# Performance work log

Hardware: AMD Instinct MI355X
Metric: run time of the kernel (lower is better)

The kernel has to match this reference:

```python
import jax, jax.numpy as jnp
import numpy as np

LEAK = 0.01  # PyTorch LeakyReLU default negative_slope


def _leaky(x):
    return jnp.where(x >= 0, x, LEAK * x)


def _sim1(x, ws):
    # 7-layer 1x1-conv MLP applied per pixel; x: (..., Cin, H, W)
    n = len(ws)
    for i, w in enumerate(ws):
        x = jnp.einsum('oc,...chw->...ohw', w, x)
        if i < n - 1:
            x = _leaky(x)
    return x


def setup_inputs() -> dict:
    key = jax.random.key(0)
    ks = jax.random.split(key, 9)
    B, C, S, K = 8, 256, 15, 17
    d = {
        'template_feature': jax.random.normal(ks[0], (B, C, S, S), jnp.float32),
        'candidate_feature': jax.random.normal(ks[1], (B, C, S + K - 1, S + K - 1), jnp.float32),
    }
    chans = [(C, 2 * C), (C // 2, C), (C // 4, C // 2), (C // 8, C // 4),
             (C // 16, C // 8), (C // 32, C // 16), (1, C // 32)]
    for i, (o, c) in enumerate(chans):
        # kaiming_normal_ fan_out for a 1x1 conv: std = sqrt(2/out_channels)
        d[f'w{i}'] = jax.random.normal(ks[2 + i], (o, c), jnp.float32) * np.sqrt(2.0 / o).astype(np.float32)
    return d


def reference(template_feature, candidate_feature, w0, w1, w2, w3, w4, w5, w6):
    ws = (w0, w1, w2, w3, w4, w5, w6)
    B, C, S, _ = template_feature.shape
    K = 17  # sliding-window grid (31-15+1)

    # ---- template branch ----
    t_mean = jnp.mean(template_feature, axis=(-2, -1), keepdims=True)
    rep = jnp.concatenate([jnp.broadcast_to(t_mean, template_feature.shape),
                           template_feature], axis=1)  # (B, 2C, S, S)
    w = _sim1(rep, ws)  # (B, 1, S, S)
    wn = jax.nn.softmax(w.reshape(B, 1, -1), axis=2).reshape(B, 1, S, S)
    common_template = jnp.sum(template_feature * wn, axis=(-2, -1)).reshape(B, C, 1, 1)

    # ---- candidate branch: im2col of 15x15 windows over 31x31 -> 17x17 grid ----
    ii = jnp.arange(S)[:, None] + jnp.arange(K)[None, :]  # (S, K): in-window + window-offset
    # cand_all[b,c,i,j,p,q] = candidate[b,c, i+p, j+q]  -> (B, C, S, S, K, K)
    cand_all = candidate_feature[:, :, ii[:, None, :, None], ii[None, :, None, :]]
    c_mean = jnp.mean(cand_all, axis=(2, 3), keepdims=True)  # divide by S*S as in original
    rep_c = jnp.concatenate([jnp.broadcast_to(c_mean, cand_all.shape), cand_all], axis=1)  # (B, 2C, S, S, K, K)
    rep_c = jnp.transpose(rep_c, (0, 4, 5, 1, 2, 3))  # (B, K, K, 2C, S, S)
    w_c = _sim1(rep_c, ws)  # (B, K, K, 1, S, S)
    wcn = jax.nn.softmax(w_c.reshape(B, K, K, 1, -1), axis=-1).reshape(B, K, K, 1, S, S)
    wcn = jnp.transpose(wcn, (0, 3, 4, 5, 1, 2))  # (B, 1, S, S, K, K)
    common_candidate = jnp.sum(cand_all * wcn, axis=(2, 3))  # (B, C, K, K)

    return common_template, common_candidate
```

## Files before the change

kernel.cpp:

```cpp
#include <hip/hip_runtime.h>

typedef _Float16 half_t;
typedef half_t half4 __attribute__((ext_vector_type(4)));
typedef half_t half8 __attribute__((ext_vector_type(8)));
typedef __fp16 pk16x2 __attribute__((ext_vector_type(2)));
typedef float  f32x4 __attribute__((ext_vector_type(4)));
typedef float  f32x2 __attribute__((ext_vector_type(2)));

static __device__ __forceinline__ half4 pack4(f32x4 a) {
  pk16x2 lo = __builtin_amdgcn_cvt_pkrtz(a[0], a[1]);
  pk16x2 hi = __builtin_amdgcn_cvt_pkrtz(a[2], a[3]);
  half4 h;
  h[0] = lo[0]; h[1] = lo[1]; h[2] = hi[0]; h[3] = hi[1];
  return h;
}

constexpr int B_  = 8;
constexpr int S_  = 15;
constexpr int K_  = 17;
constexpr int P_  = 31;
constexpr int SS_ = 225;
constexpr int PP_ = 961;
constexpr int KK_ = 289;

constexpr int NROW_C = B_ * PP_;
constexpr int NROW_T = B_ * SS_;
constexpr int NROW   = NROW_C + NROW_T;

constexpr int NW0H = 512 * 256;
constexpr int NF16 = 128*256 + 64*128 + 32*64;

constexpr size_t OFF_IN   = 0;
constexpr size_t OFF_OUT0 = OFF_IN   + (size_t)NROW * 256;
constexpr size_t OFF_ROWS = OFF_OUT0 + (size_t)NROW * 512;
constexpr size_t OFF_M0   = OFF_ROWS + (size_t)B_ * 31 * 17 * 256;
constexpr size_t OFF_TM0  = OFF_M0   + (size_t)B_ * KK_ * 256;
constexpr size_t OFF_F16  = OFF_TM0  + (size_t)B_ * 256;

constexpr int X0B  = 0;
constexpr int X1B  = 32768;
constexpr int X3TB = 32768;
constexpr int Y4B  = 41984;
constexpr int SMB  = 49152;
constexpr int REDB = 50112;
constexpr int W4B  = 50176;
constexpr int W5B  = 52480;
constexpr int W6B  = 53120;
constexpr int ROWB = 53152;
constexpr int LDSB = 53632;

__global__ __launch_bounds__(256) void featT_kernel(
    const float* __restrict__ templ, const float* __restrict__ cand,
    float* __restrict__ inarr)
{
  __shared__ float tile[32 * 257];
  const int bid = blockIdx.x;
  const float* src;
  int base, npos, rowbase;
  if (bid < B_ * 31) {
    int b = bid / 31, ch = bid % 31;
    src = cand + (size_t)b * 256 * PP_;
    base = ch * 32; npos = min(32, PP_ - base);
    rowbase = b * PP_ + base;
  } else {
    int t = bid - B_ * 31;
    int b = t / 8, ch = t % 8;
    src = templ + (size_t)b * 256 * SS_;
    base = ch * 32; npos = min(32, SS_ - base);
    rowbase = NROW_C + b * SS_ + base;
  }
  const int tid = threadIdx.x;
  const int p  = tid & 31;
  const int c8 = tid >> 5;
  const int stride = (bid < B_ * 31) ? PP_ : SS_;
  if (p < npos) {
    for (int it = 0; it < 32; ++it) {
      int c = c8 * 32 + it;
      tile[p * 257 + c] = src[(size_t)c * stride + base + p];
    }
  }
  __syncthreads();
  for (int pp = 0; pp < npos; ++pp)
    inarr[(size_t)(rowbase + pp) * 256 + tid] = tile[pp * 257 + tid];
}

__global__ __launch_bounds__(256) void wcvt_kernel(
    const float* __restrict__ w0, const float* __restrict__ w1,
    const float* __restrict__ w2, const float* __restrict__ w3,
    half_t* __restrict__ w0h, half_t* __restrict__ w1h,
    half_t* __restrict__ w2h, half_t* __restrict__ w3h)
{
  const int total = NW0H + NF16;
  for (int idx = blockIdx.x * blockDim.x + threadIdx.x; idx < total;
       idx += gridDim.x * blockDim.x) {
    if (idx < NW0H) {
      int m = idx >> 8; int c = idx & 255;
      w0h[idx] = (half_t)(m < 256 ? w0[m * 512 + 256 + c] : w0[(m - 256) * 512 + c]);
    } else {
      int t = idx - NW0H;
      if (t < 32768)      w1h[t] = (half_t)w1[t];
      else if (t < 40960) w2h[t - 32768] = (half_t)w2[t - 32768];
      else                w3h[t - 40960] = (half_t)w3[t - 40960];
    }
  }
}

__global__ __launch_bounds__(512) void l0gemm_kernel(
    const float* __restrict__ in, const half_t* __restrict__ w0h,
    float* __restrict__ out0)
{
  __shared__ __align__(16) char xls[16 * 512];
  const int tid  = threadIdx.x;
  const int lane = tid & 63;
  const int wvs  = tid >> 6;
  const int row0 = blockIdx.x * 16;

  {
    const int row = tid >> 5;
    const int c8  = (tid & 31) * 8;
    const float* src = in + (size_t)(row0 + row) * 256 + c8;
    half8 h;
#pragma unroll
    for (int r = 0; r < 8; ++r) h[r] = (half_t)src[r];
    const int off = (row * 512 + c8 * 2) ^ ((row & 7) << 4);
    *(half8*)(xls + off) = h;
  }
  __syncthreads();

  const int l15 = lane & 15, g = lane >> 4;
  f32x4 acc[4];
#pragma unroll
  for (int mt = 0; mt < 4; ++mt) acc[mt] = (f32x4){0.f, 0.f, 0.f, 0.f};
#pragma unroll 2
  for (int kb = 0; kb < 8; ++kb) {
    const int off = (l15 * 512 + kb * 64 + g * 16) ^ ((l15 & 7) << 4);
    half8 bfr = *(const half8*)(xls + off);
#pragma unroll
    for (int mt = 0; mt < 4; ++mt) {
      const half_t* ap = w0h + (size_t)((wvs * 4 + mt) * 16 + l15) * 256 + kb * 32 + g * 8;
      half8 a = *(const half8*)ap;
      acc[mt] = __builtin_amdgcn_mfma_f32_16x16x32_f16(a, bfr, acc[mt], 0, 0, 0);
    }
  }
#pragma unroll
  for (int mt = 0; mt < 4; ++mt) {
    const int m0c = (wvs * 4 + mt) * 16 + g * 4;
    *(f32x4*)(out0 + (size_t)(row0 + l15) * 512 + m0c) = acc[mt];
  }
}

__global__ __launch_bounds__(256) void rowsum_kernel(
    const float* __restrict__ out0, float* __restrict__ rows)
{
  const int bid = blockIdx.x;
  const int o = threadIdx.x;
  const int v = bid % 17; const int p = (bid / 17) % 31; const int b = bid / (17 * 31);
  float s = 0.f;
  for (int j = 0; j < 15; ++j)
    s += out0[(size_t)(b * PP_ + p * P_ + v + j) * 512 + 256 + o];
  rows[(size_t)bid * 256 + o] = s;
}

__global__ __launch_bounds__(256) void colsum_kernel(
    const float* __restrict__ rows, float* __restrict__ m0v)
{
  const int bid = blockIdx.x;
  const int o = threadIdx.x;
  const int v = bid % 17; const int u = (bid / 17) % 17; const int b = bid / KK_;
  float s = 0.f;
  for (int i = 0; i < 15; ++i)
    s += rows[(size_t)((b * 31 + u + i) * 17 + v) * 256 + o];
  m0v[(size_t)bid * 256 + o] = s * (1.0f / 225.0f);
}

__global__ __launch_bounds__(256) void tmean0_kernel(
    const float* __restrict__ out0, float* __restrict__ tm0v)
{
  const int b = blockIdx.x;
  const int o = threadIdx.x;
  float s = 0.f;
  for (int t = 0; t < SS_; ++t)
    s += out0[(size_t)(NROW_C + b * SS_ + t) * 512 + 256 + o];
  tm0v[b * 256 + o] = s * (1.0f / 225.0f);
}

__global__ __launch_bounds__(512, 4) void chain_kernel(
    const float* __restrict__ out0, const float* __restrict__ m0v,
    const float* __restrict__ tm0v,
    const half_t* __restrict__ w1h, const half_t* __restrict__ w2h,
    const half_t* __restrict__ w3h,
    const float* __restrict__ w4, const float* __restrict__ w5,
    const float* __restrict__ w6,
    const float* __restrict__ inarr, float* __restrict__ out)
{
  __shared__ __align__(16) char lds[LDSB];
  float*    ldsf   = (float*)lds;
  float*    sm     = (float*)(lds + SMB);
  float*    red    = (float*)(lds + REDB);
  uint16_t* rowoff = (uint16_t*)(lds + ROWB);

  const int tid  = threadIdx.x;
  const int lane = tid & 63;
  const int wvs  = __builtin_amdgcn_readfirstlane(tid >> 6);
  const int bid  = (blockIdx.x & 7) * 290 + (blockIdx.x >> 3);
  const bool is_t = (bid >= B_ * KK_);
  int b, u = 0, v = 0;
  const float* mean_vec;
  if (!is_t) {
    b = bid / KK_;
    int r = bid % KK_;
    u = r / K_; v = r % K_;
    mean_vec = m0v + (size_t)bid * 256;
  } else {
    b = bid - B_ * KK_;
    mean_vec = tm0v + (size_t)b * 256;
  }

  if (tid < SS_) {
    int i = tid / 15, j = tid - i * 15;
    rowoff[tid] = is_t ? (uint16_t)(NROW_C + b * SS_ + tid)
                       : (uint16_t)(b * PP_ + (u + i) * P_ + (v + j));
  }
  ((float*)(lds + W4B))[(tid >> 5) * 36 + (tid & 31)] = w4[tid];
  if (tid < 128) ((float*)(lds + W5B))[(tid >> 4) * 20 + (tid & 15)] = w5[tid];
  if (tid < 8)   ((float*)(lds + W6B))[tid] = w6[tid];

  const half_t* w1base = w1h + (size_t)(16 * wvs + (lane & 15)) * 256 + ((lane >> 4) << 3);
  const int g2 = wvs & 3, h2 = wvs >> 2;
  half8 af2[4];
  {
    const half_t* base = w2h + (size_t)(16 * g2 + (lane & 15)) * 128 + ((lane >> 4) << 3);
#pragma unroll
    for (int kb = 0; kb < 4; ++kb) af2[kb] = *(const half8*)(base + kb * 32);
  }
  const int rt3 = wvs & 1, ct3 = wvs >> 1;
  const half_t* b3ptr = w3h + (size_t)(16 * rt3 + (lane & 15)) * 64 + ((lane >> 4) << 3);
  const int c8  = (lane & 31) * 8;
  const int lhi = lane >> 5;
  const f32x4 mv8a = *(const f32x4*)(mean_vec + c8);
  const f32x4 mv8b = *(const f32x4*)(mean_vec + c8 + 4);
  __syncthreads();

  for (int ti = 0; ti < 4; ++ti) {
    const int s0 = ti * 64;
    const int cnt = min(64, SS_ - s0);

    for (int it = 0; it < 4; ++it) {
      const int pos = 8 * wvs + it * 2 + lhi;
      const int srow = rowoff[min(s0 + pos, SS_ - 1)];
      f32x4 xa = *(const f32x4*)(out0 + ((size_t)srow << 9) + c8);
      f32x4 xb = *(const f32x4*)(out0 + ((size_t)srow << 9) + c8 + 4);
      f32x4 a0, a1;
#pragma unroll
      for (int r = 0; r < 4; ++r) {
        float t2 = xa[r] + mv8a[r];
        a0[r] = fmaxf(t2, 0.01f * t2);
        float t3 = xb[r] + mv8b[r];
        a1[r] = fmaxf(t3, 0.01f * t3);
      }
      half4 h0 = pack4(a0), h1 = pack4(a1);
      half8 h8;
#pragma unroll
      for (int r = 0; r < 4; ++r) { h8[r] = h0[r]; h8[4 + r] = h1[r]; }
      const int off = (pos * 512 + c8 * 2) ^ ((pos & 7) << 4);
      *(half8*)(lds + X0B + off) = h8;
    }
    __syncthreads();

    f32x4 acc[4];
#pragma unroll
    for (int nt = 0; nt < 4; ++nt) acc[nt] = (f32x4){0.f, 0.f, 0.f, 0.f};
    {
      const half_t* w1p = w1base;
      asm volatile("" : "+v"(w1p));
#pragma unroll 2
      for (int kb = 0; kb < 8; ++kb) {
        half8 a1 = *(const half8*)(w1p + kb * 32);
        const int kbyte = kb * 64 + ((lane >> 4) << 4);
#pragma unroll
        for (int nt = 0; nt < 4; ++nt) {
          const int pos = nt * 16 + (lane & 15);
          const int off = (pos * 512 + kbyte) ^ ((pos & 7) << 4);
          half8 bfr = *(const half8*)(lds + X0B + off);
          acc[nt] = __builtin_amdgcn_mfma_f32_16x16x32_f16(a1, bfr, acc[nt], 0, 0, 0);
        }
      }
#pragma unroll
      for (int nt = 0; nt < 4; ++nt) {
        const int pos = nt * 16 + (lane & 15);
        f32x4 a;
#pragma unroll
        for (int r = 0; r < 4; ++r) a[r] = fmaxf(acc[nt][r], 0.01f * acc[nt][r]);
        const int ch0 = 16 * wvs + ((lane >> 4) << 2);
        const int off = (pos * 256 + ch0 * 2) ^ ((pos & 7) << 4);
        *(half4*)(lds + X1B + off) = pack4(a);
      }
    }
    __syncthreads();

    f32x4 acc2[2];
#pragma unroll
    for (int nt = 0; nt < 2; ++nt) acc2[nt] = (f32x4){0.f, 0.f, 0.f, 0.f};
#pragma unroll
    for (int kb = 0; kb < 4; ++kb) {
      const int kbyte = kb * 64 + ((lane >> 4) << 4);
#pragma unroll
      for (int nt = 0; nt < 2; ++nt) {
        const int pos = h2 * 32 + nt * 16 + (lane & 15);
        const int off = (pos * 256 + kbyte) ^ ((pos & 7) << 4);
        half8 bfr = *(const half8*)(lds + X1B + off);
        acc2[nt] = __builtin_amdgcn_mfma_f32_16x16x32_f16(af2[kb], bfr, acc2[nt], 0, 0, 0);
      }
    }
#pragma unroll
    for (int nt = 0; nt < 2; ++nt) {
      const int pos = h2 * 32 + nt * 16 + (lane & 15);
      const int ch0 = 16 * g2 + ((lane >> 4) << 2);
      f32x4 a;
#pragma unroll
      for (int r = 0; r < 4; ++r) a[r] = fmaxf(acc2[nt][r], 0.01f * acc2[nt][r]);
      const int off = (pos * 128 + ch0 * 2) ^ ((pos & 7) << 4);
      *(half4*)(lds + X0B + off) = pack4(a);
    }
    __syncthreads();

    {
      f32x4 acc3 = (f32x4){0.f, 0.f, 0.f, 0.f};
      const int pos = ct3 * 16 + (lane & 15);
#pragma unroll
      for (int kb = 0; kb < 2; ++kb) {
        half8 a3 = *(const half8*)(b3ptr + kb * 32);
        const int kbyte = kb * 64 + ((lane >> 4) << 4);
        const int off = (pos * 128 + kbyte) ^ ((pos & 7) << 4);
        half8 bfr = *(const half8*)(lds + X0B + off);
        acc3 = __builtin_amdgcn_mfma_f32_16x16x32_f16(a3, bfr, acc3, 0, 0, 0);
      }
      const int ch0 = 16 * rt3 + ((lane >> 4) << 2);
      f32x4 o4;
#pragma unroll
      for (int r = 0; r < 4; ++r) o4[r] = fmaxf(acc3[r], 0.01f * acc3[r]);
      *(f32x4*)(lds + X3TB + pos * 144 + ch0 * 4) = o4;
    }
    __syncthreads();

    {
      const int p = lane >> 3, g = lane & 7;
      const int pos = 8 * wvs + p;
      float a4_0 = 0.f, a4_1 = 0.f;
#pragma unroll
      for (int c0 = 0; c0 < 32; c0 += 4) {
        f32x4 x  = *(const f32x4*)(lds + X3TB + pos * 144 + c0 * 4);
        f32x4 wA = *(const f32x4*)(lds + W4B + (2 * g) * 144 + c0 * 4);
        f32x4 wB = *(const f32x4*)(lds + W4B + (2 * g + 1) * 144 + c0 * 4);
#pragma unroll
        for (int r = 0; r < 4; ++r) {
          a4_0 = fmaf(wA[r], x[r], a4_0);
          a4_1 = fmaf(wB[r], x[r], a4_1);
        }
      }
      f32x2 y4v;
      y4v[0] = fmaxf(a4_0, 0.01f * a4_0);
      y4v[1] = fmaxf(a4_1, 0.01f * a4_1);
      *(f32x2*)(lds + Y4B + pos * 80 + g * 8) = y4v;
      float a5 = 0.f;
#pragma unroll
      for (int c0 = 0; c0 < 16; c0 += 4) {
        f32x4 x = *(const f32x4*)(lds + Y4B + pos * 80 + c0 * 4);
        f32x4 w = *(const f32x4*)(lds + W5B + g * 80 + c0 * 4);
#pragma unroll
        for (int r = 0; r < 4; ++r) a5 = fmaf(w[r], x[r], a5);
      }
      a5 = fmaxf(a5, 0.01f * a5);
      float t6 = ((float*)(lds + W6B))[g] * a5;
      t6 += __shfl_xor(t6, 1);
      t6 += __shfl_xor(t6, 2);
      t6 += __shfl_xor(t6, 4);
      if (g == 0 && (8 * wvs + p) < cnt) sm[s0 + pos] = t6;
    }
    __syncthreads();
  }

  float vv = (tid < SS_) ? sm[tid] : -1e30f;
  float m = vv;
#pragma unroll
  for (int off = 32; off >= 1; off >>= 1) m = fmaxf(m, __shfl_xor(m, off));
  if (lane == 0) red[wvs] = m;
  __syncthreads();
  m = red[0];
#pragma unroll
  for (int w = 1; w < 8; ++w) m = fmaxf(m, red[w]);
  float e = (tid < SS_) ? __expf(vv - m) : 0.f;
  float ss = e;
#pragma unroll
  for (int off = 32; off >= 1; off >>= 1) ss += __shfl_xor(ss, off);
  __syncthreads();
  if (lane == 0) red[wvs] = ss;
  __syncthreads();
  float Stot = red[0];
#pragma unroll
  for (int w = 1; w < 8; ++w) Stot += red[w];
  if (tid < SS_) sm[tid] = e / Stot;
  __syncthreads();

  {
    const int c2 = (tid & 127) * 2;
    const int q  = tid >> 7;
    float accx = 0.f, accy = 0.f;
    for (int s = q; s < SS_; s += 4) {
      f32x2 ft = *(const f32x2*)(inarr + ((size_t)rowoff[s] << 8) + c2);
      float w = sm[s];
      accx = fmaf(w, ft[0], accx);
      accy = fmaf(w, ft[1], accy);
    }
    __syncthreads();
    ldsf[q * 256 + c2]     = accx;
    ldsf[q * 256 + c2 + 1] = accy;
    __syncthreads();
    if (tid < 256) {
      float tot = ldsf[tid] + ldsf[256 + tid] + ldsf[512 + tid] + ldsf[768 + tid];
      if (!is_t) out[2048 + ((size_t)(b * 256 + tid) * 17 + u) * 17 + v] = tot;
      else       out[b * 256 + tid] = tot;
    }
  }
}

extern "C" void kernel_launch(void* const* d_in, const int* in_sizes, int n_in,
                              void* d_out, int out_size, void* d_ws, size_t ws_size,
                              hipStream_t stream)
{
  const float* templ = (const float*)d_in[0];
  const float* cand  = (const float*)d_in[1];
  const float* w0 = (const float*)d_in[2];
  const float* w1 = (const float*)d_in[3];
  const float* w2 = (const float*)d_in[4];
  const float* w3 = (const float*)d_in[5];
  const float* w4 = (const float*)d_in[6];
  const float* w5 = (const float*)d_in[7];
  const float* w6 = (const float*)d_in[8];

  float* ws    = (float*)d_ws;
  float* inarr = ws + OFF_IN;
  float* out0  = ws + OFF_OUT0;
  float* rows  = ws + OFF_ROWS;
  float* m0v   = ws + OFF_M0;
  float* tm0v  = ws + OFF_TM0;
  half_t* w0h  = (half_t*)(ws + OFF_F16);
  half_t* w1h  = w0h + NW0H;
  half_t* w2h  = w1h + 128 * 256;
  half_t* w3h  = w2h + 64 * 128;
  float* outf  = (float*)d_out;

  featT_kernel<<<B_ * 31 + B_ * 8, 256, 0, stream>>>(templ, cand, inarr);
  wcvt_kernel<<<256, 256, 0, stream>>>(w0, w1, w2, w3, w0h, w1h, w2h, w3h);
  l0gemm_kernel<<<NROW / 16, 512, 0, stream>>>(inarr, w0h, out0);
  rowsum_kernel<<<B_ * 31 * 17, 256, 0, stream>>>(out0, rows);
  colsum_kernel<<<B_ * KK_, 256, 0, stream>>>(rows, m0v);
  tmean0_kernel<<<B_, 256, 0, stream>>>(out0, tm0v);
  chain_kernel<<<B_ * KK_ + B_, 512, 0, stream>>>(out0, m0v, tm0v,
                                                  w1h, w2h, w3h, w4, w5, w6,
                                                  inarr, outf);
}
```

Measured before the change: 277.0 us.

## Store input features and conv1 activations in fp16 to halve gather traffic

The transposed input array and the first half of the layer-0 GEMM output (the per-pixel part) are now stored as fp16 instead of fp32. The mean-path half stays fp32 in a separate compact buffer used by the window sums. The chain kernel gathers fp16 conv1 rows, adds the mean and applies LeakyReLU in packed half arithmetic. It also reads the fp16 features for the final weighted sum. This aims to cut the heavy repeated global gathers in the chain kernel, at the cost of extra rounding of the inputs and of the pre-activation sums.

After: 269.0 us. 2.9% less time.

```diff
diff --git a/kernel.cpp b/kernel.cpp
--- a/kernel.cpp
+++ b/kernel.cpp
@@ -1,6 +1,7 @@
 #include <hip/hip_runtime.h>
 
 typedef _Float16 half_t;
+typedef half_t h2    __attribute__((ext_vector_type(2)));
 typedef half_t half4 __attribute__((ext_vector_type(4)));
 typedef half_t half8 __attribute__((ext_vector_type(8)));
 typedef __fp16 pk16x2 __attribute__((ext_vector_type(2)));
@@ -30,9 +31,8 @@
 constexpr int NW0H = 512 * 256;
 constexpr int NF16 = 128*256 + 64*128 + 32*64;
 
-constexpr size_t OFF_IN   = 0;
-constexpr size_t OFF_OUT0 = OFF_IN   + (size_t)NROW * 256;
-constexpr size_t OFF_ROWS = OFF_OUT0 + (size_t)NROW * 512;
+constexpr size_t OFF_GOUT = 0;
+constexpr size_t OFF_ROWS = OFF_GOUT + (size_t)NROW * 256;
 constexpr size_t OFF_M0   = OFF_ROWS + (size_t)B_ * 31 * 17 * 256;
 constexpr size_t OFF_TM0  = OFF_M0   + (size_t)B_ * KK_ * 256;
 constexpr size_t OFF_F16  = OFF_TM0  + (size_t)B_ * 256;
@@ -51,7 +51,7 @@
 
 __global__ __launch_bounds__(256) void featT_kernel(
     const float* __restrict__ templ, const float* __restrict__ cand,
-    float* __restrict__ inarr)
+    half_t* __restrict__ inarrh)
 {
   __shared__ float tile[32 * 257];
   const int bid = blockIdx.x;
@@ -81,7 +81,7 @@
   }
   __syncthreads();
   for (int pp = 0; pp < npos; ++pp)
-    inarr[(size_t)(rowbase + pp) * 256 + tid] = tile[pp * 257 + tid];
+    inarrh[(size_t)(rowbase + pp) * 256 + tid] = (half_t)tile[pp * 257 + tid];
 }
 
 __global__ __launch_bounds__(256) void wcvt_kernel(
@@ -106,8 +106,8 @@
 }
 
 __global__ __launch_bounds__(512) void l0gemm_kernel(
-    const float* __restrict__ in, const half_t* __restrict__ w0h,
-    float* __restrict__ out0)
+    const half_t* __restrict__ inh, const half_t* __restrict__ w0h,
+    half_t* __restrict__ conv1h, float* __restrict__ gout)
 {
   __shared__ __align__(16) char xls[16 * 512];
   const int tid  = threadIdx.x;
@@ -118,10 +118,7 @@
   {
     const int row = tid >> 5;
     const int c8  = (tid & 31) * 8;
-    const float* src = in + (size_t)(row0 + row) * 256 + c8;
-    half8 h;
-#pragma unroll
-    for (int r = 0; r < 8; ++r) h[r] = (half_t)src[r];
+    half8 h = *(const half8*)(inh + (size_t)(row0 + row) * 256 + c8);
     const int off = (row * 512 + c8 * 2) ^ ((row & 7) << 4);
     *(half8*)(xls + off) = h;
   }
@@ -145,19 +142,22 @@
 #pragma unroll
   for (int mt = 0; mt < 4; ++mt) {
     const int m0c = (wvs * 4 + mt) * 16 + g * 4;
-    *(f32x4*)(out0 + (size_t)(row0 + l15) * 512 + m0c) = acc[mt];
+    if (wvs < 4)
+      *(half4*)(conv1h + (size_t)(row0 + l15) * 256 + m0c) = pack4(acc[mt]);
+    else
+      *(f32x4*)(gout + (size_t)(row0 + l15) * 256 + (m0c - 256)) = acc[mt];
   }
 }
 
 __global__ __launch_bounds__(256) void rowsum_kernel(
-    const float* __restrict__ out0, float* __restrict__ rows)
+    const float* __restrict__ gout, float* __restrict__ rows)
 {
   const int bid = blockIdx.x;
   const int o = threadIdx.x;
   const int v = bid % 17; const int p = (bid / 17) % 31; const int b = bid / (17 * 31);
   float s = 0.f;
   for (int j = 0; j < 15; ++j)
-    s += out0[(size_t)(b * PP_ + p * P_ + v + j) * 512 + 256 + o];
+    s += gout[(size_t)(b * PP_ + p * P_ + v + j) * 256 + o];
   rows[(size_t)bid * 256 + o] = s;
 }
 
@@ -174,24 +174,24 @@
 }
 
 __global__ __launch_bounds__(256) void tmean0_kernel(
-    const float* __restrict__ out0, float* __restrict__ tm0v)
+    const float* __restrict__ gout, float* __restrict__ tm0v)
 {
   const int b = blockIdx.x;
   const int o = threadIdx.x;
   float s = 0.f;
   for (int t = 0; t < SS_; ++t)
-    s += out0[(size_t)(NROW_C + b * SS_ + t) * 512 + 256 + o];
+    s += gout[(size_t)(NROW_C + b * SS_ + t) * 256 + o];
   tm0v[b * 256 + o] = s * (1.0f / 225.0f);
 }
 
 __global__ __launch_bounds__(512, 4) void chain_kernel(
-    const float* __restrict__ out0, const float* __restrict__ m0v,
+    const half_t* __restrict__ conv1h, const float* __restrict__ m0v,
     const float* __restrict__ tm0v,
     const half_t* __restrict__ w1h, const half_t* __restrict__ w2h,
     const half_t* __restrict__ w3h,
     const float* __restrict__ w4, const float* __restrict__ w5,
     const float* __restrict__ w6,
-    const float* __restrict__ inarr, float* __restrict__ out)
+    const half_t* __restrict__ inarrh, float* __restrict__ out)
 {
   __shared__ __align__(16) char lds[LDSB];
   float*    ldsf   = (float*)lds;
@@ -226,7 +226,7 @@
   if (tid < 8)   ((float*)(lds + W6B))[tid] = w6[tid];
 
   const half_t* w1base = w1h + (size_t)(16 * wvs + (lane & 15)) * 256 + ((lane >> 4) << 3);
-  const int g2 = wvs & 3, h2 = wvs >> 2;
+  const int g2 = wvs & 3, h2w = wvs >> 2;
   half8 af2[4];
   {
     const half_t* base = w2h + (size_t)(16 * g2 + (lane & 15)) * 128 + ((lane >> 4) << 3);
@@ -237,8 +237,14 @@
   const half_t* b3ptr = w3h + (size_t)(16 * rt3 + (lane & 15)) * 64 + ((lane >> 4) << 3);
   const int c8  = (lane & 31) * 8;
   const int lhi = lane >> 5;
-  const f32x4 mv8a = *(const f32x4*)(mean_vec + c8);
-  const f32x4 mv8b = *(const f32x4*)(mean_vec + c8 + 4);
+  half8 mvh;
+  {
+    f32x4 ma = *(const f32x4*)(mean_vec + c8);
+    f32x4 mb = *(const f32x4*)(mean_vec + c8 + 4);
+    half4 h0 = pack4(ma), h1 = pack4(mb);
+#pragma unroll
+    for (int r = 0; r < 4; ++r) { mvh[r] = h0[r]; mvh[4 + r] = h1[r]; }
+  }
   __syncthreads();
 
   for (int ti = 0; ti < 4; ++ti) {
@@ -248,22 +254,12 @@
     for (int it = 0; it < 4; ++it) {
       const int pos = 8 * wvs + it * 2 + lhi;
       const int srow = rowoff[min(s0 + pos, SS_ - 1)];
-      f32x4 xa = *(const f32x4*)(out0 + ((size_t)srow << 9) + c8);
-      f32x4 xb = *(const f32x4*)(out0 + ((size_t)srow << 9) + c8 + 4);
-      f32x4 a0, a1;
-#pragma unroll
-      for (int r = 0; r < 4; ++r) {
-        float t2 = xa[r] + mv8a[r];
-        a0[r] = fmaxf(t2, 0.01f * t2);
-        float t3 = xb[r] + mv8b[r];
-        a1[r] = fmaxf(t3, 0.01f * t3);
-      }
-      half4 h0 = pack4(a0), h1 = pack4(a1);
-      half8 h8;
-#pragma unroll
-      for (int r = 0; r < 4; ++r) { h8[r] = h0[r]; h8[4 + r] = h1[r]; }
+      half8 cv = *(const half8*)(conv1h + ((size_t)srow << 8) + c8);
+      half8 t = cv + mvh;
+      half8 s2 = t * (half_t)0.01f;
+      half8 r8 = __builtin_elementwise_max(t, s2);
       const int off = (pos * 512 + c8 * 2) ^ ((pos & 7) << 4);
-      *(half8*)(lds + X0B + off) = h8;
+      *(half8*)(lds + X0B + off) = r8;
     }
     __syncthreads();
 
@@ -306,7 +302,7 @@
       const int kbyte = kb * 64 + ((lane >> 4) << 4);
 #pragma unroll
       for (int nt = 0; nt < 2; ++nt) {
-        const int pos = h2 * 32 + nt * 16 + (lane & 15);
+        const int pos = h2w * 32 + nt * 16 + (lane & 15);
         const int off = (pos * 256 + kbyte) ^ ((pos & 7) << 4);
         half8 bfr = *(const half8*)(lds + X1B + off);
         acc2[nt] = __builtin_amdgcn_mfma_f32_16x16x32_f16(af2[kb], bfr, acc2[nt], 0, 0, 0);
@@ -314,7 +310,7 @@
     }
 #pragma unroll
     for (int nt = 0; nt < 2; ++nt) {
-      const int pos = h2 * 32 + nt * 16 + (lane & 15);
+      const int pos = h2w * 32 + nt * 16 + (lane & 15);
       const int ch0 = 16 * g2 + ((lane >> 4) << 2);
       f32x4 a;
 #pragma unroll
@@ -407,10 +403,10 @@
     const int q  = tid >> 7;
     float accx = 0.f, accy = 0.f;
     for (int s = q; s < SS_; s += 4) {
-      f32x2 ft = *(const f32x2*)(inarr + ((size_t)rowoff[s] << 8) + c2);
+      h2 ft = *(const h2*)(inarrh + ((size_t)rowoff[s] << 8) + c2);
       float w = sm[s];
-      accx = fmaf(w, ft[0], accx);
-      accy = fmaf(w, ft[1], accy);
+      accx = fmaf(w, (float)ft[0], accx);
+      accy = fmaf(w, (float)ft[1], accy);
     }
     __syncthreads();
     ldsf[q * 256 + c2]     = accx;
@@ -439,24 +435,25 @@
   const float* w6 = (const float*)d_in[8];
 
   float* ws    = (float*)d_ws;
-  float* inarr = ws + OFF_IN;
-  float* out0  = ws + OFF_OUT0;
+  float* gout  = ws + OFF_GOUT;
   float* rows  = ws + OFF_ROWS;
   float* m0v   = ws + OFF_M0;
   float* tm0v  = ws + OFF_TM0;
-  half_t* w0h  = (half_t*)(ws + OFF_F16);
+  half_t* inarrh = (half_t*)(ws + OFF_F16);
+  half_t* conv1h = inarrh + (size_t)NROW * 256;
+  half_t* w0h  = conv1h + (size_t)NROW * 256;
   half_t* w1h  = w0h + NW0H;
   half_t* w2h  = w1h + 128 * 256;
   half_t* w3h  = w2h + 64 * 128;
   float* outf  = (float*)d_out;
 
-  featT_kernel<<<B_ * 31 + B_ * 8, 256, 0, stream>>>(templ, cand, inarr);
+  featT_kernel<<<B_ * 31 + B_ * 8, 256, 0, stream>>>(templ, cand, inarrh);
   wcvt_kernel<<<256, 256, 0, stream>>>(w0, w1, w2, w3, w0h, w1h, w2h, w3h);
-  l0gemm_kernel<<<NROW / 16, 512, 0, stream>>>(inarr, w0h, out0);
-  rowsum_kernel<<<B_ * 31 * 17, 256, 0, stream>>>(out0, rows);
+  l0gemm_kernel<<<NROW / 16, 512, 0, stream>>>(inarrh, w0h, conv1h, gout);
+  rowsum_kernel<<<B_ * 31 * 17, 256, 0, stream>>>(gout, rows);
   colsum_kernel<<<B_ * KK_, 256, 0, stream>>>(rows, m0v);
-  tmean0_kernel<<<B_, 256, 0, stream>>>(out0, tm0v);
-  chain_kernel<<<B_ * KK_ + B_, 512, 0, stream>>>(out0, m0v, tm0v,
+  tmean0_kernel<<<B_, 256, 0, stream>>>(gout, tm0v);
+  chain_kernel<<<B_ * KK_ + B_, 512, 0, stream>>>(conv1h, m0v, tm0v,
                                                   w1h, w2h, w3h, w4, w5, w6,
-                                                  inarr, outf);
-}
+                                                  inarrh, outf);
+}
```
